# Kernel optimization log

Hardware: AMD Instinct MI355X
Metric: run time of the kernel (lower is better)

Reference implementation:

```python
import jax, jax.numpy as jnp
import numpy as np

B, P, T = 64, 8400, 100


def _corners(b):
    # b: [..., 4] in (cx, cy, w, h) -> (x1, y1, x2, y2)
    cx, cy, w, h = b[..., 0], b[..., 1], b[..., 2], b[..., 3]
    return cx - w / 2, cy - h / 2, cx + w / 2, cy + h / 2


def _pairwise_iou(pred_box, tgt_box):
    # pred_box: [B, P, 4], tgt_box: [B, T, 4] -> iou [B, T, P]
    px1, py1, px2, py2 = _corners(pred_box[:, None, :, :])   # [B,1,P]
    tx1, ty1, tx2, ty2 = _corners(tgt_box[:, :, None, :])    # [B,T,1]
    ix1 = jnp.maximum(px1, tx1)
    iy1 = jnp.maximum(py1, ty1)
    ix2 = jnp.minimum(px2, tx2)
    iy2 = jnp.minimum(py2, ty2)
    inter = jnp.maximum(ix2 - ix1, 0.0) * jnp.maximum(iy2 - iy1, 0.0)
    area_p = (px2 - px1) * (py2 - py1)
    area_t = (tx2 - tx1) * (ty2 - ty1)
    return inter / (area_p + area_t - inter + 1e-6)


def setup_inputs() -> dict:
    key = jax.random.key(0)
    k1, k2, k3 = jax.random.split(key, 3)
    predictions = jax.random.uniform(k1, (B, P, 5), dtype=jnp.float32)
    targets = jax.random.uniform(k2, (B, T, 5), dtype=jnp.float32)
    lengths = jax.random.randint(k3, (B,), 0, T, dtype=jnp.int64)
    return {"predictions": predictions, "targets": targets, "lengths": lengths}


def reference(predictions, targets, lengths):
    # predictions: [B, P, 5], targets: [B, T, 5], lengths: [B]
    iou = _pairwise_iou(predictions[..., 1:], targets[..., 1:])  # [B, T, P]
    # strict '>' in original keeps first max; argmax also returns first occurrence
    best_idx = jnp.argmax(iou, axis=-1)                          # [B, T]
    matched = jnp.take_along_axis(predictions, best_idx[..., None], axis=1)  # [B, T, 5]
    sq = jnp.sum((matched - targets) ** 2, axis=-1)              # [B, T]
    valid = jnp.arange(targets.shape[1]) < lengths[:, None]      # [B, T]
    loss = jnp.sum(jnp.where(valid, sq, 0.0)) / predictions.shape[0]
    return loss
```

## Files before the change

kernel.cpp:

```cpp
#include <hip/hip_runtime.h>

#define BB 64
#define PP 8400
#define TT 100
#define TG 5
#define NGRP (TT / TG)
#define NSPLIT 2
#define NBLK (BB * NGRP * NSPLIT)
#define NGROUPS8 (PP / 8)
#define GRPH (NGROUPS8 / NSPLIT)
#define NE (BB * TT)

__global__ __launch_bounds__(256) void yolo_match_kernel(
    const float* __restrict__ pred,
    const float* __restrict__ tgt,
    float*       __restrict__ wsbest,
    int*         __restrict__ wsidx)
{
#pragma clang fp contract(off)
    const int blkraw = blockIdx.x;
    const int x    = blkraw & 7;
    const int r    = blkraw >> 3;
    const int bhi  = r / (NGRP * NSPLIT);
    const int rem  = r - bhi * (NGRP * NSPLIT);
    const int grp  = rem / NSPLIT;
    const int half = rem - grp * NSPLIT;
    const int b    = x + 8 * bhi;
    const int t0   = grp * TG;
    const int tid  = threadIdx.x;
    const int lane = tid & 63;
    const int wid  = tid >> 6;

    const float*  pb  = pred + (size_t)b * PP * 5;
    const float4* pb4 = (const float4*)pb;
    const float*  tb  = tgt + ((size_t)b * TT + t0) * 5;

    float tx1[TG], ty1[TG], tx2[TG], ty2[TG], ta[TG];
#pragma unroll
    for (int g = 0; g < TG; ++g) {
        const float tcx = tb[g * 5 + 1], tcy = tb[g * 5 + 2];
        const float tw  = tb[g * 5 + 3], th  = tb[g * 5 + 4];
        tx1[g] = tcx - tw * 0.5f;
        ty1[g] = tcy - th * 0.5f;
        tx2[g] = tcx + tw * 0.5f;
        ty2[g] = tcy + th * 0.5f;
        ta[g]  = (tx2[g] - tx1[g]) * (ty2[g] - ty1[g]);
    }

    float best[TG];
    int   bidx[TG];
#pragma unroll
    for (int g = 0; g < TG; ++g) { best[g] = -1.0f; bidx[g] = 0; }

    const int gbeg = half * GRPH;
    const int gend = gbeg + GRPH;
    for (int g0 = gbeg + tid; g0 < gend; g0 += 256) {
        float4 q[10];
#pragma unroll
        for (int k = 0; k < 10; ++k) q[k] = pb4[g0 * 10 + k];

        float cxs[8], cys[8], wss[8], hss[8];
#pragma unroll
        for (int h = 0; h < 2; ++h) {
            const float4 v0 = q[5 * h + 0];
            const float4 v1 = q[5 * h + 1];
            const float4 v2 = q[5 * h + 2];
            const float4 v3 = q[5 * h + 3];
            const float4 v4 = q[5 * h + 4];
            cxs[4 * h + 0] = v0.y; cys[4 * h + 0] = v0.z; wss[4 * h + 0] = v0.w; hss[4 * h + 0] = v1.x;
            cxs[4 * h + 1] = v1.z; cys[4 * h + 1] = v1.w; wss[4 * h + 1] = v2.x; hss[4 * h + 1] = v2.y;
            cxs[4 * h + 2] = v2.w; cys[4 * h + 2] = v3.x; wss[4 * h + 2] = v3.y; hss[4 * h + 2] = v3.z;
            cxs[4 * h + 3] = v4.x; cys[4 * h + 3] = v4.y; wss[4 * h + 3] = v4.z; hss[4 * h + 3] = v4.w;
        }

#pragma unroll
        for (int j = 0; j < 8; ++j) {
            const float px1 = cxs[j] - wss[j] * 0.5f;
            const float py1 = cys[j] - hss[j] * 0.5f;
            const float px2 = cxs[j] + wss[j] * 0.5f;
            const float py2 = cys[j] + hss[j] * 0.5f;
            const float area_p = (px2 - px1) * (py2 - py1);
            const int   p = g0 * 8 + j;

#pragma unroll
            for (int g = 0; g < TG; ++g) {
                const float ix1 = fmaxf(px1, tx1[g]);
                const float iy1 = fmaxf(py1, ty1[g]);
                const float ix2 = fminf(px2, tx2[g]);
                const float iy2 = fminf(py2, ty2[g]);
                const float inter = fmaxf(ix2 - ix1, 0.0f) * fmaxf(iy2 - iy1, 0.0f);
                const float denom = ((area_p + ta[g]) - inter) + 1e-6f;
                const float iou   = inter / denom;
                if (iou > best[g]) { best[g] = iou; bidx[g] = p; }
            }
        }
    }

    __shared__ float s_best[4][TG];
    __shared__ int   s_bidx[4][TG];

#pragma unroll
    for (int g = 0; g < TG; ++g) {
        float bv = best[g];
        int   bi = bidx[g];
        for (int off = 32; off > 0; off >>= 1) {
            const float ob = __shfl_down(bv, off, 64);
            const int   oi = __shfl_down(bi, off, 64);
            if (ob > bv || (ob == bv && oi < bi)) { bv = ob; bi = oi; }
        }
        if (lane == 0) { s_best[wid][g] = bv; s_bidx[wid][g] = bi; }
    }
    __syncthreads();

    if (tid < TG) {
        const int g = tid;
        float bv = s_best[0][g];
        int   bi = s_bidx[0][g];
#pragma unroll
        for (int w = 1; w < 4; ++w) {
            const float ob = s_best[w][g];
            const int   oi = s_bidx[w][g];
            if (ob > bv || (ob == bv && oi < bi)) { bv = ob; bi = oi; }
        }
        const int e = ((b * TT + t0 + g) << 1) | half;
        wsbest[e] = bv;
        wsidx[e]  = bi;
    }
}

__global__ __launch_bounds__(1024) void yolo_finish_kernel(
    const float* __restrict__ pred,
    const float* __restrict__ tgt,
    const int*   __restrict__ lengths,
    const float* __restrict__ wsbest,
    const int*   __restrict__ wsidx,
    float*       __restrict__ out)
{
#pragma clang fp contract(off)
    const int tid = threadIdx.x;
    float acc = 0.0f;

    for (int e = tid; e < NE; e += 1024) {
        const int b = e / TT;
        const int t = e - b * TT;
        const float b0 = wsbest[2 * e + 0];
        const float b1 = wsbest[2 * e + 1];
        const int   i0 = wsidx[2 * e + 0];
        const int   i1 = wsidx[2 * e + 1];
        const int   bi = (b1 > b0) ? i1 : i0;

        const float* mp = pred + ((size_t)b * PP + bi) * 5;
        const float* tp = tgt  + ((size_t)b * TT + t) * 5;
        float sq = 0.0f;
        for (int k = 0; k < 5; ++k) {
            const float d = mp[k] - tp[k];
            sq += d * d;
        }
        acc += (t < lengths[b]) ? sq : 0.0f;
    }

    __shared__ float sm[1024];
    sm[tid] = acc;
    __syncthreads();
    for (int off = 512; off > 0; off >>= 1) {
        if (tid < off) sm[tid] += sm[tid + off];
        __syncthreads();
    }
    if (tid == 0) out[0] = sm[0] / (float)BB;
}

extern "C" void kernel_launch(void* const* d_in, const int* in_sizes, int n_in,
                              void* d_out, int out_size, void* d_ws, size_t ws_size,
                              hipStream_t stream) {
    const float* pred    = (const float*)d_in[0];
    const float* tgt     = (const float*)d_in[1];
    const int*   lengths = (const int*)d_in[2];
    float* out = (float*)d_out;

    float* wsbest = (float*)d_ws;
    int*   wsidx  = (int*)d_ws + NE * NSPLIT;

    yolo_match_kernel<<<NBLK, 256, 0, stream>>>(pred, tgt, wsbest, wsidx);
    yolo_finish_kernel<<<1, 1024, 0, stream>>>(pred, tgt, lengths,
                                               wsbest, wsidx, out);
}
```

Baseline: 119.2 us.

## Replace IoU division with cross-multiplied comparison and drop prediction split

The per-pair division inter/denom is replaced by tracking the best numerator and denominator and comparing by cross-multiplication, which removes the costly float divide from the inner loop. The two-way split of predictions across blocks is also removed, so each block scans all predictions for its five targets and only the winning index is written to workspace. This halves the block count, which may reduce occupancy and latency hiding. Cross-multiplication rounds differently from true division, so near-ties can select a different index than the reference.

```diff
diff --git a/kernel.cpp b/kernel.cpp
--- a/kernel.cpp
+++ b/kernel.cpp
@@ -5,26 +5,20 @@
 #define TT 100
 #define TG 5
 #define NGRP (TT / TG)
-#define NSPLIT 2
-#define NBLK (BB * NGRP * NSPLIT)
-#define NGROUPS8 (PP / 8)
-#define GRPH (NGROUPS8 / NSPLIT)
+#define NBLK (BB * NGRP)
 #define NE (BB * TT)
 
 __global__ __launch_bounds__(256) void yolo_match_kernel(
     const float* __restrict__ pred,
     const float* __restrict__ tgt,
-    float*       __restrict__ wsbest,
     int*         __restrict__ wsidx)
 {
 #pragma clang fp contract(off)
     const int blkraw = blockIdx.x;
     const int x    = blkraw & 7;
     const int r    = blkraw >> 3;
-    const int bhi  = r / (NGRP * NSPLIT);
-    const int rem  = r - bhi * (NGRP * NSPLIT);
-    const int grp  = rem / NSPLIT;
-    const int half = rem - grp * NSPLIT;
+    const int bhi  = r / NGRP;
+    const int grp  = r - bhi * NGRP;
     const int b    = x + 8 * bhi;
     const int t0   = grp * TG;
     const int tid  = threadIdx.x;
@@ -47,14 +41,12 @@
         ta[g]  = (tx2[g] - tx1[g]) * (ty2[g] - ty1[g]);
     }
 
-    float best[TG];
+    float bn[TG], bd[TG];
     int   bidx[TG];
 #pragma unroll
-    for (int g = 0; g < TG; ++g) { best[g] = -1.0f; bidx[g] = 0; }
+    for (int g = 0; g < TG; ++g) { bn[g] = 0.0f; bd[g] = 1e30f; bidx[g] = 0; }
 
-    const int gbeg = half * GRPH;
-    const int gend = gbeg + GRPH;
-    for (int g0 = gbeg + tid; g0 < gend; g0 += 256) {
+    for (int g0 = tid; g0 < PP / 8; g0 += 256) {
         float4 q[10];
 #pragma unroll
         for (int k = 0; k < 10; ++k) q[k] = pb4[g0 * 10 + k];
@@ -90,41 +82,47 @@
                 const float iy2 = fminf(py2, ty2[g]);
                 const float inter = fmaxf(ix2 - ix1, 0.0f) * fmaxf(iy2 - iy1, 0.0f);
                 const float denom = ((area_p + ta[g]) - inter) + 1e-6f;
-                const float iou   = inter / denom;
-                if (iou > best[g]) { best[g] = iou; bidx[g] = p; }
+                const float lhs = inter * bd[g];
+                const float rhs = bn[g] * denom;
+                if (lhs > rhs) { bn[g] = inter; bd[g] = denom; bidx[g] = p; }
             }
         }
     }
 
-    __shared__ float s_best[4][TG];
-    __shared__ int   s_bidx[4][TG];
+    __shared__ float s_bn[4][TG];
+    __shared__ float s_bd[4][TG];
+    __shared__ int   s_bi[4][TG];
 
 #pragma unroll
     for (int g = 0; g < TG; ++g) {
-        float bv = best[g];
-        int   bi = bidx[g];
+        float n = bn[g], d = bd[g];
+        int   i = bidx[g];
         for (int off = 32; off > 0; off >>= 1) {
-            const float ob = __shfl_down(bv, off, 64);
-            const int   oi = __shfl_down(bi, off, 64);
-            if (ob > bv || (ob == bv && oi < bi)) { bv = ob; bi = oi; }
+            const float on = __shfl_down(n, off, 64);
+            const float od = __shfl_down(d, off, 64);
+            const int   oi = __shfl_down(i, off, 64);
+            const float lhs = on * d;
+            const float rhs = n * od;
+            if (lhs > rhs || (lhs == rhs && oi < i)) { n = on; d = od; i = oi; }
         }
-        if (lane == 0) { s_best[wid][g] = bv; s_bidx[wid][g] = bi; }
+        if (lane == 0) { s_bn[wid][g] = n; s_bd[wid][g] = d; s_bi[wid][g] = i; }
     }
     __syncthreads();
 
     if (tid < TG) {
         const int g = tid;
-        float bv = s_best[0][g];
-        int   bi = s_bidx[0][g];
+        float n = s_bn[0][g], d = s_bd[0][g];
+        int   i = s_bi[0][g];
 #pragma unroll
         for (int w = 1; w < 4; ++w) {
-            const float ob = s_best[w][g];
-            const int   oi = s_bidx[w][g];
-            if (ob > bv || (ob == bv && oi < bi)) { bv = ob; bi = oi; }
+            const float on = s_bn[w][g];
+            const float od = s_bd[w][g];
+            const int   oi = s_bi[w][g];
+            const float lhs = on * d;
+            const float rhs = n * od;
+            if (lhs > rhs || (lhs == rhs && oi < i)) { n = on; d = od; i = oi; }
         }
-        const int e = ((b * TT + t0 + g) << 1) | half;
-        wsbest[e] = bv;
-        wsidx[e]  = bi;
+        wsidx[b * TT + t0 + g] = i;
     }
 }
 
@@ -132,7 +130,6 @@
     const float* __restrict__ pred,
     const float* __restrict__ tgt,
     const int*   __restrict__ lengths,
-    const float* __restrict__ wsbest,
     const int*   __restrict__ wsidx,
     float*       __restrict__ out)
 {
@@ -143,14 +140,10 @@
     for (int e = tid; e < NE; e += 1024) {
         const int b = e / TT;
         const int t = e - b * TT;
-        const float b0 = wsbest[2 * e + 0];
-        const float b1 = wsbest[2 * e + 1];
-        const int   i0 = wsidx[2 * e + 0];
-        const int   i1 = wsidx[2 * e + 1];
-        const int   bi = (b1 > b0) ? i1 : i0;
+        const int bi = wsidx[e];
 
         const float* mp = pred + ((size_t)b * PP + bi) * 5;
-        const float* tp = tgt  + ((size_t)b * TT + t) * 5;
+        const float* tp = tgt  + (size_t)e * 5;
         float sq = 0.0f;
         for (int k = 0; k < 5; ++k) {
             const float d = mp[k] - tp[k];
@@ -176,11 +169,8 @@
     const float* tgt     = (const float*)d_in[1];
     const int*   lengths = (const int*)d_in[2];
     float* out = (float*)d_out;
+    int*   wsidx = (int*)d_ws;
 
-    float* wsbest = (float*)d_ws;
-    int*   wsidx  = (int*)d_ws + NE * NSPLIT;
-
-    yolo_match_kernel<<<NBLK, 256, 0, stream>>>(pred, tgt, wsbest, wsidx);
-    yolo_finish_kernel<<<1, 1024, 0, stream>>>(pred, tgt, lengths,
-                                               wsbest, wsidx, out);
+    yolo_match_kernel<<<NBLK, 256, 0, stream>>>(pred, tgt, wsidx);
+    yolo_finish_kernel<<<1, 1024, 0, stream>>>(pred, tgt, lengths, wsidx, out);
 }
```

Result: faster. 109.2 us (-8.3%).
